# Kernel optimization log

Hardware: AMD Instinct MI355X
Metric: run time of the kernel (lower is better)

Reference implementation:

```python
import jax, jax.numpy as jnp
import numpy as np

B, L, D, H = 8, 1024, 768, 12
HD = D // H
EPS = 1e-5
R_EPS = 1e-12  # numerical guard for r at coincident positions


def setup_inputs() -> dict:
    key = jax.random.key(0)
    ks = jax.random.split(key, 8)
    x = jax.random.normal(ks[0], (B, L, D), dtype=jnp.float32)
    # 32x32 patch grid coordinates, same for every batch element
    g = jnp.arange(32, dtype=jnp.float32)
    yy, xx = jnp.meshgrid(g, g, indexing='ij')
    pos = jnp.broadcast_to(jnp.stack([yy.ravel(), xx.ravel()], axis=-1), (B, L, 2))
    w_norm = jnp.ones((D,), dtype=jnp.float32)
    w_in = 0.02 * jax.random.normal(ks[1], (3 * D, D), dtype=jnp.float32)
    b_in = jnp.zeros((3 * D,), dtype=jnp.float32)
    w_out = 0.02 * jax.random.normal(ks[2], (D, D), dtype=jnp.float32)
    b_out = jnp.zeros((D,), dtype=jnp.float32)
    # bias params [H, 6] = (o, c, w, p, delta, m) per init_bias_params
    o = jnp.zeros((H,), dtype=jnp.float32)
    c = 1.0 + 0.3 * jax.random.uniform(ks[3], (H,), dtype=jnp.float32)
    w = jnp.ones((H,), dtype=jnp.float32)
    p = jnp.zeros((H,), dtype=jnp.float32)
    delta = jax.random.normal(ks[4], (H,), dtype=jnp.float32)
    m = jnp.ones((H,), dtype=jnp.float32)
    bias_params = jnp.stack([o, c, w, p, delta, m], axis=-1)
    return {"x": x, "pos": pos, "w_norm": w_norm, "w_in": w_in, "b_in": b_in,
            "w_out": w_out, "b_out": b_out, "bias_params": bias_params}


def _bias_grid(pos, bias_params):
    # pos: [B, L, 2] -> bias: [B, H, L, L]
    o, c, w, p, delta, m = [bias_params[:, i].reshape(1, H, 1, 1) for i in range(6)]
    dist = pos[:, :, None, :] - pos[:, None, :, :]          # [B, Lq, Lk, 2]
    theta = jnp.arctan2(dist[..., 1], dist[..., 0])[:, None]  # [B, 1, Lq, Lk]
    r = jnp.sqrt(jnp.sum(dist * dist, axis=-1) + R_EPS)[:, None]
    term1 = jax.nn.relu(r - o) ** jnp.abs(c)
    term2 = 1.0 - jnp.abs(jnp.tanh(delta)) * (jnp.cos((theta - p) * w * 0.5) ** 2) ** jnp.abs(m)
    return term1 * term2


def reference(x, pos, w_norm, w_in, b_in, w_out, b_out, bias_params):
    bias = _bias_grid(pos, bias_params)                      # [B, H, L, L]
    # RMSNorm
    xn = x * jax.lax.rsqrt(jnp.mean(x * x, axis=-1, keepdims=True) + EPS) * w_norm
    qkv = xn @ w_in.T + b_in                                 # [B, L, 3D]
    q, k, v = jnp.split(qkv, 3, axis=-1)
    def heads(t):
        return t.reshape(B, L, H, HD).transpose(0, 2, 1, 3)  # [B, H, L, HD]
    q, k, v = heads(q), heads(k), heads(v)
    scores = jnp.einsum('bhqd,bhkd->bhqk', q, k) / jnp.sqrt(jnp.float32(HD)) + bias
    attn = jax.nn.softmax(scores, axis=-1)
    o = jnp.einsum('bhqk,bhkd->bhqd', attn, v)
    o = o.transpose(0, 2, 1, 3).reshape(B, L, D)
    return o @ w_out.T + b_out
```

## Files before the change

### kernel.cpp

```cpp
#include <hip/hip_runtime.h>

#define BB 8
#define LL 1024
#define DD 768
#define HH 12
#define HD 64

typedef short s16x8 __attribute__((ext_vector_type(8)));
typedef float f32x4 __attribute__((ext_vector_type(4)));

static __device__ __forceinline__ unsigned short f2bf(float f){
  unsigned int u = __builtin_bit_cast(unsigned int, f);
  u = (u + 0x7FFFu + ((u >> 16) & 1u)) >> 16;
  return (unsigned short)u;
}

static __device__ __forceinline__ unsigned int pk_bf(float a, float b){
  unsigned int ua = __builtin_bit_cast(unsigned int, a) + 0x8000u;
  unsigned int ub = __builtin_bit_cast(unsigned int, b) + 0x8000u;
  return __builtin_amdgcn_perm(ub, ua, 0x07060302);
}

static __device__ __forceinline__ f32x4 mfma16(s16x8 a, s16x8 b, f32x4 c){
  return __builtin_amdgcn_mfma_f32_16x16x32_bf16(a, b, c, 0, 0, 0);
}

static __device__ __forceinline__ void gld_lds16(const void* g, void* l){
  __builtin_amdgcn_global_load_lds(
      (const __attribute__((address_space(1))) void*)g,
      (__attribute__((address_space(3))) void*)l, 16, 0, 0);
}

__global__ void cvt_kernel(const float* __restrict__ src, unsigned short* __restrict__ dst, int n4){
  int i = blockIdx.x*256 + threadIdx.x;
  if (i < n4){
    float4 v = ((const float4*)src)[i];
    ushort4 o;
    o.x = f2bf(v.x); o.y = f2bf(v.y); o.z = f2bf(v.z); o.w = f2bf(v.w);
    ((ushort4*)dst)[i] = o;
  }
}

__global__ void bias_table_kernel(const float* __restrict__ bp, float* __restrict__ table){
  int idx = blockIdx.x*256 + threadIdx.x;
  if (idx >= HH*3969) return;
  int hh = idx/3969, rem = idx - hh*3969;
  int dy = rem/63 - 31, dx = rem%63 - 31;
  float o  = bp[hh*6+0], c = bp[hh*6+1], w = bp[hh*6+2];
  float p  = bp[hh*6+3], dl = bp[hh*6+4], m = bp[hh*6+5];
  float theta = atan2f((float)dx, (float)dy);
  float r = sqrtf((float)(dy*dy + dx*dx) + 1e-12f);
  float t1 = powf(fmaxf(r - o, 0.0f), fabsf(c));
  float co = cosf((theta - p)*w*0.5f);
  float t2 = 1.0f - fabsf(tanhf(dl))*powf(co*co, fabsf(m));
  table[idx] = t1*t2*1.44269504f;
}

__global__ __launch_bounds__(64) void bmax_kernel(const float* __restrict__ table,
                                                  float* __restrict__ bmax){
  int qy = blockIdx.x, h = blockIdx.y;
  __shared__ float m1[63];
  int t = threadIdx.x;
  const float* tb = table + h*3969;
  if (t < 63){
    float m = -3.0e38f;
    #pragma unroll 4
    for (int row = qy; row < qy + 32; row++) m = fmaxf(m, tb[row*63 + t]);
    m1[t] = m;
  }
  __syncthreads();
  if (t < 32){
    float m = -3.0e38f;
    #pragma unroll 4
    for (int c = t; c < t + 32; c++) m = fmaxf(m, m1[c]);
    bmax[(h*32 + qy)*32 + t] = m;
  }
}

__global__ __launch_bounds__(256) void rmsnorm_kernel(const float* __restrict__ x,
                                                      const float* __restrict__ wn,
                                                      unsigned short* __restrict__ xn){
  int row = blockIdx.x, t = threadIdx.x;
  const float* xr = x + (size_t)row*DD;
  float v0 = xr[t], v1 = xr[t+256], v2 = xr[t+512];
  float ss = v0*v0 + v1*v1 + v2*v2;
  #pragma unroll
  for (int m = 1; m < 64; m <<= 1) ss += __shfl_xor(ss, m, 64);
  __shared__ float red[4];
  if ((t & 63) == 0) red[t >> 6] = ss;
  __syncthreads();
  float tot = red[0] + red[1] + red[2] + red[3];
  float sc = rsqrtf(tot*(1.0f/DD) + 1e-5f);
  unsigned short* xo = xn + (size_t)row*DD;
  xo[t]     = f2bf(v0*sc*wn[t]);
  xo[t+256] = f2bf(v1*sc*wn[t+256]);
  xo[t+512] = f2bf(v2*sc*wn[t+512]);
}

static __device__ __forceinline__ void storeC(float* p, float v){ *p = v; }
static __device__ __forceinline__ void storeC(unsigned short* p, float v){ *p = f2bf(v); }

template<int MODE, int TN, typename OutT>
__global__ __launch_bounds__(256) void gemm_bt_kernel(const unsigned short* __restrict__ A,
                                                      const unsigned short* __restrict__ B,
                                                      const float* __restrict__ bias,
                                                      OutT* __restrict__ C,
                                                      unsigned short* __restrict__ qp,
                                                      unsigned short* __restrict__ kp,
                                                      unsigned short* __restrict__ vp,
                                                      int M, int N, int K){
  constexpr int NT = TN/32;
  __shared__ __align__(16) unsigned short As[2][128*32];
  __shared__ __align__(16) unsigned short Bs[2][TN*32];
  int tid = threadIdx.x;
  int w = tid >> 6, lane = tid & 63, quad = lane >> 4, col = lane & 15;
  int wm = (w >> 1)*64, wn = (w & 1)*(TN/2);
  int bm = blockIdx.x*128, bn = blockIdx.y*TN;

  int srow = lane >> 2;
  int schunk = (lane & 3)*8;
  const unsigned short* ga0 = A + (size_t)(bm + w*32 + srow)*K + schunk;
  const unsigned short* ga1 = ga0 + (size_t)16*K;
  const unsigned short* gb0 = B + (size_t)(bn + w*(TN/4) + srow)*K + schunk;
  const unsigned short* gb1 = gb0 + (size_t)16*K;

  f32x4 acc[4][NT];
  #pragma unroll
  for (int mt = 0; mt < 4; mt++)
    #pragma unroll
    for (int nt = 0; nt < NT; nt++) acc[mt][nt] = (f32x4){0.f,0.f,0.f,0.f};

  gld_lds16(ga0, As[0] + (w*32)*32);
  gld_lds16(ga1, As[0] + (w*32 + 16)*32);
  gld_lds16(gb0, Bs[0] + (w*(TN/4))*32);
  if (TN == 128) gld_lds16(gb1, Bs[0] + (w*32 + 16)*32);

  int KT = K >> 5;
  for (int t = 0; t < KT; t++){
    int buf = t & 1;
    __syncthreads();
    if (t + 1 < KT){
      int kk = (t + 1)*32;
      gld_lds16(ga0 + kk, As[buf^1] + (w*32)*32);
      gld_lds16(ga1 + kk, As[buf^1] + (w*32 + 16)*32);
      gld_lds16(gb0 + kk, Bs[buf^1] + (w*(TN/4))*32);
      if (TN == 128) gld_lds16(gb1 + kk, Bs[buf^1] + (w*32 + 16)*32);
    }
    s16x8 af[4], bf[NT];
    #pragma unroll
    for (int mt = 0; mt < 4; mt++)
      af[mt] = *(const s16x8*)&As[buf][(wm + mt*16 + col)*32 + quad*8];
    #pragma unroll
    for (int nt = 0; nt < NT; nt++)
      bf[nt] = *(const s16x8*)&Bs[buf][(wn + nt*16 + col)*32 + quad*8];
    #pragma unroll
    for (int mt = 0; mt < 4; mt++)
      #pragma unroll
      for (int nt = 0; nt < NT; nt++)
        acc[mt][nt] = mfma16(af[mt], bf[nt], acc[mt][nt]);
  }

  #pragma unroll
  for (int mt = 0; mt < 4; mt++)
    #pragma unroll
    for (int nt = 0; nt < NT; nt++){
      int cl = bn + wn + nt*16 + col;
      float bv = bias[cl];
      #pragma unroll
      for (int r = 0; r < 4; r++){
        int rw = bm + wm + mt*16 + quad*4 + r;
        float v = acc[mt][nt][r] + bv;
        if (MODE == 0){
          storeC(&C[(size_t)rw*N + cl], v);
        } else {
          int part = cl >= 1536 ? 2 : (cl >= 768 ? 1 : 0);
          int hd = cl - part*768;
          int h = hd >> 6, d = hd & 63;
          int bb = rw >> 10, l = rw & 1023;
          size_t base = (((size_t)bb*HH + h)*LL + l)*64;
          unsigned short v16 = f2bf(v);
          if (part == 0)      qp[base + d] = v16;
          else if (part == 1) kp[base + ((((d>>3) ^ (l&7)) << 3) | (d & 7))] = v16;
          else                vp[base + d] = v16;
        }
      }
    }
}

__global__ __launch_bounds__(256) void vtrans_kernel(const unsigned short* __restrict__ vp,
                                                     unsigned short* __restrict__ vt2){
  int jt = blockIdx.x, bh = blockIdx.y;
  __shared__ unsigned short tile[32][68];
  int t = threadIdx.x;
  const unsigned short* src = vp + ((size_t)bh*LL + jt*32)*64;
  #pragma unroll
  for (int e = 0; e < 8; e++){
    int lin = t + 256*e;
    tile[lin >> 6][lin & 63] = src[lin];
  }
  __syncthreads();
  unsigned short* dst = vt2 + ((size_t)bh*32 + jt)*2048;
  #pragma unroll
  for (int e = 0; e < 8; e++){
    int lin = t + 256*e;
    dst[lin] = tile[lin & 31][lin >> 5];
  }
}

__global__ __launch_bounds__(256) void attn_kernel(const unsigned short* __restrict__ qp,
                                                   const unsigned short* __restrict__ kp,
                                                   const unsigned short* __restrict__ vt2,
                                                   const float* __restrict__ table,
                                                   const float* __restrict__ bmax,
                                                   const float* __restrict__ pos,
                                                   unsigned short* __restrict__ o_out){
  int i = blockIdx.x;
  int bh = (i >> 6)*8 + (i & 7);
  int qt = (i >> 3) & 7;
  int b = bh/HH, h = bh - b*HH;
  int tid = threadIdx.x, w = tid >> 6, lane = tid & 63, quad = lane >> 4, col = lane & 15;
  __shared__ float tl[3969];
  __shared__ int ky63[32];
  __shared__ __align__(16) unsigned short Ks[2][2048];
  __shared__ __align__(16) unsigned short Vs[2][2048];
  __shared__ __align__(16) unsigned short ps[4][2][16][40];

  const unsigned short* kgp = kp  + (size_t)bh*65536;
  const unsigned short* vgp = vt2 + (size_t)bh*65536;
  int soff = w*512 + lane*8;

  gld_lds16(kgp + soff, &Ks[0][w*512]);
  gld_lds16(vgp + soff, &Vs[0][w*512]);

  for (int j = tid; j < 3969; j += 256) tl[j] = table[h*3969 + j];
  const float* pb = pos + (size_t)b*2048;
  if (tid < 32) ky63[tid] = 63*__float2int_rn(pb[tid*64]);
  __syncthreads();

  int qw = qt*128 + w*32;
  const unsigned short* qpb = qp + (size_t)bh*65536;
  s16x8 qa[2][2];
  int cq[2];
  float mh[2];
  #pragma unroll
  for (int g = 0; g < 2; g++){
    int q = qw + g*16 + col;
    size_t qo = (size_t)q*64 + quad*8;
    qa[g][0] = *(const s16x8*)(qpb + qo);
    qa[g][1] = *(const s16x8*)(qpb + qo + 32);
    int qy = __float2int_rn(pb[q*2]);
    int qx = __float2int_rn(pb[q*2 + 1]);
    cq[g] = qy*63 + qx + 1984 - quad*4;
    mh[g] = bmax[(h*32 + qy)*32 + qx];
  }

  int sw = col & 7;
  int a_k0 = col*128 + ((quad    ) ^ sw)*16;
  int a_k1 = col*128 + ((quad + 4) ^ sw)*16;
  int a_k2 = a_k0 + 2048;
  int a_k3 = a_k1 + 2048;
  int a_v  = col*64 + quad*16;

  f32x4 o[2][4];
  #pragma unroll
  for (int g = 0; g < 2; g++)
    #pragma unroll
    for (int nt = 0; nt < 4; nt++) o[g][nt] = (f32x4){0.f,0.f,0.f,0.f};
  float l_run[2] = {0.0f, 0.0f};

  for (int t = 0; t < 32; t++){
    int buf = t & 1;
    __syncthreads();
    if (t < 31){
      gld_lds16(kgp + (t+1)*2048 + soff, &Ks[buf^1][w*512]);
      gld_lds16(vgp + (t+1)*2048 + soff, &Vs[buf^1][w*512]);
    }
    const char* kb = (const char*)Ks[buf];
    const char* vb = (const char*)Vs[buf];
    s16x8 k0 = *(const s16x8*)(kb + a_k0);
    s16x8 k1 = *(const s16x8*)(kb + a_k1);
    s16x8 k2 = *(const s16x8*)(kb + a_k2);
    s16x8 k3 = *(const s16x8*)(kb + a_k3);
    s16x8 v0 = *(const s16x8*)(vb + a_v);
    s16x8 v1 = *(const s16x8*)(vb + a_v + 1024);
    s16x8 v2 = *(const s16x8*)(vb + a_v + 2048);
    s16x8 v3 = *(const s16x8*)(vb + a_v + 3072);
    int kyt = ky63[t];

    f32x4 z = {0.f,0.f,0.f,0.f};
    #pragma unroll
    for (int g = 0; g < 2; g++){
      f32x4 s_lo = mfma16(k0, qa[g][0], z);  s_lo = mfma16(k1, qa[g][1], s_lo);
      f32x4 s_hi = mfma16(k2, qa[g][0], z);  s_hi = mfma16(k3, qa[g][1], s_hi);
      int base = cq[g] - kyt;
      float pl[4], ph[4];
      #pragma unroll
      for (int r = 0; r < 4; r++){
        float svl = __builtin_fmaf(s_lo[r], 0.18033688f, tl[base - r]      - mh[g]);
        float svh = __builtin_fmaf(s_hi[r], 0.18033688f, tl[base - r - 16] - mh[g]);
        pl[r] = exp2f(svl);
        ph[r] = exp2f(svh);
      }
      l_run[g] += ((pl[0]+pl[1]) + (pl[2]+pl[3]) + (ph[0]+ph[1]) + (ph[2]+ph[3]));
      unsigned short* pw = &ps[w][g][col][0];
      *(unsigned int*)&pw[quad*4]      = pk_bf(pl[0], pl[1]);
      *(unsigned int*)&pw[quad*4 + 2]  = pk_bf(pl[2], pl[3]);
      *(unsigned int*)&pw[quad*4 + 16] = pk_bf(ph[0], ph[1]);
      *(unsigned int*)&pw[quad*4 + 18] = pk_bf(ph[2], ph[3]);
    }

    #pragma unroll
    for (int g = 0; g < 2; g++){
      s16x8 pf = *(const s16x8*)((const char*)&ps[w][g][col][0] + quad*16);
      o[g][0] = mfma16(v0, pf, o[g][0]);
      o[g][1] = mfma16(v1, pf, o[g][1]);
      o[g][2] = mfma16(v2, pf, o[g][2]);
      o[g][3] = mfma16(v3, pf, o[g][3]);
    }
  }

  #pragma unroll
  for (int g = 0; g < 2; g++){
    float lr = l_run[g];
    lr += __shfl_xor(lr, 16, 64);
    lr += __shfl_xor(lr, 32, 64);
    float inv = 1.0f / lr;
    int q = qw + g*16 + col;
    unsigned short* orow = o_out + (size_t)(b*LL + q)*DD + h*64;
    #pragma unroll
    for (int nt = 0; nt < 4; nt++){
      uint2 pkd;
      pkd.x = pk_bf(o[g][nt][0]*inv, o[g][nt][1]*inv);
      pkd.y = pk_bf(o[g][nt][2]*inv, o[g][nt][3]*inv);
      *(uint2*)&orow[nt*16 + quad*4] = pkd;
    }
  }
}

extern "C" void kernel_launch(void* const* d_in, const int* in_sizes, int n_in,
                              void* d_out, int out_size, void* d_ws, size_t ws_size,
                              hipStream_t stream){
  const float* x      = (const float*)d_in[0];
  const float* pos    = (const float*)d_in[1];
  const float* w_norm = (const float*)d_in[2];
  const float* w_in   = (const float*)d_in[3];
  const float* b_in   = (const float*)d_in[4];
  const float* w_out  = (const float*)d_in[5];
  const float* b_out  = (const float*)d_in[6];
  const float* bp     = (const float*)d_in[7];

  char* ws = (char*)d_ws;
  unsigned short* xn    = (unsigned short*)(ws);
  unsigned short* winb  = (unsigned short*)(ws + 12582912);
  unsigned short* woutb = (unsigned short*)(ws + 16121856);
  unsigned short* qpb   = (unsigned short*)(ws + 17301504);
  unsigned short* kpb   = (unsigned short*)(ws + 29884416);
  unsigned short* vpb   = (unsigned short*)(ws + 42467328);
  unsigned short* vt2b  = (unsigned short*)(ws + 55050240);
  float*          table = (float*)        (ws + 67633152);
  unsigned short* ob    = (unsigned short*)(ws + 67823664);
  float*          bmaxp = (float*)        (ws);

  cvt_kernel<<<dim3((2304*768/4)/256), dim3(256), 0, stream>>>(w_in, winb, 2304*768/4);
  cvt_kernel<<<dim3((768*768/4)/256), dim3(256), 0, stream>>>(w_out, woutb, 768*768/4);
  bias_table_kernel<<<dim3((HH*3969 + 255)/256), dim3(256), 0, stream>>>(bp, table);
  rmsnorm_kernel<<<dim3(BB*LL), dim3(256), 0, stream>>>(x, w_norm, xn);
  gemm_bt_kernel<1, 128, unsigned short><<<dim3(64, 18), dim3(256), 0, stream>>>(
      xn, winb, b_in, (unsigned short*)nullptr, qpb, kpb, vpb, BB*LL, 3*DD, DD);
  bmax_kernel<<<dim3(32, HH), dim3(64), 0, stream>>>(table, bmaxp);
  vtrans_kernel<<<dim3(32, BB*HH), dim3(256), 0, stream>>>(vpb, vt2b);
  attn_kernel<<<dim3(768), dim3(256), 0, stream>>>(qpb, kpb, vt2b, table, bmaxp, pos, ob);
  gemm_bt_kernel<0, 64, float><<<dim3(64, 12), dim3(256), 0, stream>>>(
      ob, woutb, b_out, (float*)d_out, nullptr, nullptr, nullptr, BB*LL, DD, DD);
}
```

Baseline: 244.6 us.

## Keep attention probabilities in registers via permlane swaps and MFMA row sums

Stops round-tripping the bf16 probability tile through shared memory. P fragments are now rearranged into MFMA operand layout with v_permlane32/16_swap. The row-max subtraction is folded into the score MFMA's initial accumulator, and the softmax denominator is computed by an extra MFMA against a ones vector. Packing uses the hardware v_cvt_pk_bf16_f32 instruction. Together these remove the LDS writes and reads and the scalar add chains, at the cost of one extra MFMA per group, and the denominator now sums the bf16-rounded probabilities.

Result: faster. 239.5 us (-2.1%).

```diff
diff --git a/kernel.cpp b/kernel.cpp
--- a/kernel.cpp
+++ b/kernel.cpp
@@ -8,6 +8,7 @@
 
 typedef short s16x8 __attribute__((ext_vector_type(8)));
 typedef float f32x4 __attribute__((ext_vector_type(4)));
+typedef unsigned int u32x4 __attribute__((ext_vector_type(4)));
 
 static __device__ __forceinline__ unsigned short f2bf(float f){
   unsigned int u = __builtin_bit_cast(unsigned int, f);
@@ -15,10 +16,17 @@
   return (unsigned short)u;
 }
 
-static __device__ __forceinline__ unsigned int pk_bf(float a, float b){
-  unsigned int ua = __builtin_bit_cast(unsigned int, a) + 0x8000u;
-  unsigned int ub = __builtin_bit_cast(unsigned int, b) + 0x8000u;
-  return __builtin_amdgcn_perm(ub, ua, 0x07060302);
+static __device__ __forceinline__ unsigned int cvtpk_bf(float a, float b){
+  unsigned int r;
+  asm("v_cvt_pk_bf16_f32 %0, %1, %2" : "=v"(r) : "v"(a), "v"(b));
+  return r;
+}
+
+static __device__ __forceinline__ void swap32(unsigned int& a, unsigned int& b){
+  asm("v_permlane32_swap_b32 %0, %1" : "+v"(a), "+v"(b));
+}
+static __device__ __forceinline__ void swap16(unsigned int& a, unsigned int& b){
+  asm("v_permlane16_swap_b32 %0, %1" : "+v"(a), "+v"(b));
 }
 
 static __device__ __forceinline__ f32x4 mfma16(s16x8 a, s16x8 b, f32x4 c){
@@ -223,7 +231,6 @@
   __shared__ int ky63[32];
   __shared__ __align__(16) unsigned short Ks[2][2048];
   __shared__ __align__(16) unsigned short Vs[2][2048];
-  __shared__ __align__(16) unsigned short ps[4][2][16][40];
 
   const unsigned short* kgp = kp  + (size_t)bh*65536;
   const unsigned short* vgp = vt2 + (size_t)bh*65536;
@@ -241,7 +248,7 @@
   const unsigned short* qpb = qp + (size_t)bh*65536;
   s16x8 qa[2][2];
   int cq[2];
-  float mh[2];
+  f32x4 zb[2];
   #pragma unroll
   for (int g = 0; g < 2; g++){
     int q = qw + g*16 + col;
@@ -251,8 +258,13 @@
     int qy = __float2int_rn(pb[q*2]);
     int qx = __float2int_rn(pb[q*2 + 1]);
     cq[g] = qy*63 + qx + 1984 - quad*4;
-    mh[g] = bmax[(h*32 + qy)*32 + qx];
-  }
+    float neg = -5.5451774445f * bmax[(h*32 + qy)*32 + qx];
+    zb[g] = (f32x4){neg, neg, neg, neg};
+  }
+
+  s16x8 ones;
+  #pragma unroll
+  for (int e = 0; e < 8; e++) ones[e] = (short)0x3F80;
 
   int sw = col & 7;
   int a_k0 = col*128 + ((quad    ) ^ sw)*16;
@@ -262,11 +274,13 @@
   int a_v  = col*64 + quad*16;
 
   f32x4 o[2][4];
-  #pragma unroll
-  for (int g = 0; g < 2; g++)
+  f32x4 l_acc[2];
+  #pragma unroll
+  for (int g = 0; g < 2; g++){
     #pragma unroll
     for (int nt = 0; nt < 4; nt++) o[g][nt] = (f32x4){0.f,0.f,0.f,0.f};
-  float l_run[2] = {0.0f, 0.0f};
+    l_acc[g] = (f32x4){0.f,0.f,0.f,0.f};
+  }
 
   for (int t = 0; t < 32; t++){
     int buf = t & 1;
@@ -287,31 +301,26 @@
     s16x8 v3 = *(const s16x8*)(vb + a_v + 3072);
     int kyt = ky63[t];
 
-    f32x4 z = {0.f,0.f,0.f,0.f};
     #pragma unroll
     for (int g = 0; g < 2; g++){
-      f32x4 s_lo = mfma16(k0, qa[g][0], z);  s_lo = mfma16(k1, qa[g][1], s_lo);
-      f32x4 s_hi = mfma16(k2, qa[g][0], z);  s_hi = mfma16(k3, qa[g][1], s_hi);
+      f32x4 s_lo = mfma16(k0, qa[g][0], zb[g]);  s_lo = mfma16(k1, qa[g][1], s_lo);
+      f32x4 s_hi = mfma16(k2, qa[g][0], zb[g]);  s_hi = mfma16(k3, qa[g][1], s_hi);
       int base = cq[g] - kyt;
       float pl[4], ph[4];
       #pragma unroll
       for (int r = 0; r < 4; r++){
-        float svl = __builtin_fmaf(s_lo[r], 0.18033688f, tl[base - r]      - mh[g]);
-        float svh = __builtin_fmaf(s_hi[r], 0.18033688f, tl[base - r - 16] - mh[g]);
-        pl[r] = exp2f(svl);
-        ph[r] = exp2f(svh);
+        pl[r] = exp2f(__builtin_fmaf(s_lo[r], 0.18033688f, tl[base - r]));
+        ph[r] = exp2f(__builtin_fmaf(s_hi[r], 0.18033688f, tl[base - r - 16]));
       }
-      l_run[g] += ((pl[0]+pl[1]) + (pl[2]+pl[3]) + (ph[0]+ph[1]) + (ph[2]+ph[3]));
-      unsigned short* pw = &ps[w][g][col][0];
-      *(unsigned int*)&pw[quad*4]      = pk_bf(pl[0], pl[1]);
-      *(unsigned int*)&pw[quad*4 + 2]  = pk_bf(pl[2], pl[3]);
-      *(unsigned int*)&pw[quad*4 + 16] = pk_bf(ph[0], ph[1]);
-      *(unsigned int*)&pw[quad*4 + 18] = pk_bf(ph[2], ph[3]);
-    }
-
-    #pragma unroll
-    for (int g = 0; g < 2; g++){
-      s16x8 pf = *(const s16x8*)((const char*)&ps[w][g][col][0] + quad*16);
+      unsigned int wA = cvtpk_bf(pl[0], pl[1]);
+      unsigned int wB = cvtpk_bf(pl[2], pl[3]);
+      unsigned int wC = cvtpk_bf(ph[0], ph[1]);
+      unsigned int wD = cvtpk_bf(ph[2], ph[3]);
+      swap32(wA, wC);  swap32(wB, wD);
+      swap16(wA, wC);  swap16(wB, wD);
+      u32x4 pv4; pv4.x = wA; pv4.y = wB; pv4.z = wC; pv4.w = wD;
+      s16x8 pf = __builtin_bit_cast(s16x8, pv4);
+      l_acc[g] = mfma16(ones, pf, l_acc[g]);
       o[g][0] = mfma16(v0, pf, o[g][0]);
       o[g][1] = mfma16(v1, pf, o[g][1]);
       o[g][2] = mfma16(v2, pf, o[g][2]);
@@ -321,17 +330,14 @@
 
   #pragma unroll
   for (int g = 0; g < 2; g++){
-    float lr = l_run[g];
-    lr += __shfl_xor(lr, 16, 64);
-    lr += __shfl_xor(lr, 32, 64);
-    float inv = 1.0f / lr;
+    float inv = 1.0f / l_acc[g][0];
     int q = qw + g*16 + col;
     unsigned short* orow = o_out + (size_t)(b*LL + q)*DD + h*64;
     #pragma unroll
     for (int nt = 0; nt < 4; nt++){
       uint2 pkd;
-      pkd.x = pk_bf(o[g][nt][0]*inv, o[g][nt][1]*inv);
-      pkd.y = pk_bf(o[g][nt][2]*inv, o[g][nt][3]*inv);
+      pkd.x = cvtpk_bf(o[g][nt][0]*inv, o[g][nt][1]*inv);
+      pkd.y = cvtpk_bf(o[g][nt][2]*inv, o[g][nt][3]*inv);
       *(uint2*)&orow[nt*16 + quad*4] = pkd;
     }
   }
```
